# Kernel optimization log

Measured on AMD Instinct MI355X. Metric: run time of the kernel, lower is better.

Reference implementation:

```python
import jax, jax.numpy as jnp
import numpy as np

EPS = 1e-7
STRIDE = 1
PAD = 3


def _mantissa_map(v):
    # (|v|+eps) * 2^(-floor(log2(|v|+eps))) - 1  -> mantissa-1 in [0,1)
    a = jnp.abs(v) + EPS
    base = a * jnp.exp2(-jnp.floor(jnp.log2(a))) - 1.0
    # piecewise: >=0.5 -> (1+base)/2, else 1+base  (values in [0.75, 1.5))
    return jnp.where(base >= 0.5, (1.0 + base) * 0.5, 1.0 + base)


def _unfold(x, kH, kW, stride, pad, Ho, Wo):
    # im2col matching torch.nn.Unfold ordering (kernel position index = i*kW + j)
    xp = jnp.pad(x, ((0, 0), (0, 0), (pad, pad), (pad, pad)))
    cols = [xp[:, :, i:i + stride * Ho:stride, j:j + stride * Wo:stride]
            for i in range(kH) for j in range(kW)]
    return jnp.stack(cols, axis=-1)  # (B, C, Ho, Wo, kH*kW)


def setup_inputs() -> dict:
    key = jax.random.key(0)
    k1, k2 = jax.random.split(key)
    x = jax.random.normal(k1, (4, 192, 56, 56), dtype=jnp.float32)
    weight = jax.random.normal(k2, (192, 1, 7, 7), dtype=jnp.float32) * 0.1
    return {"x": x, "weight": weight}


def reference(x, weight):
    B, C, H, W = x.shape
    _, _, kH, kW = weight.shape
    Ho = (H + 2 * PAD - kH) // STRIDE + 1
    Wo = (W + 2 * PAD - kW) // STRIDE + 1
    KK = kH * kW

    # mantissa factors
    m2 = _mantissa_map(weight).reshape(C, KK)[None, :, None, None, :]  # (1,C,1,1,KK)
    m1 = _unfold(_mantissa_map(x), kH, kW, STRIDE, PAD, Ho, Wo)        # (B,C,Ho,Wo,KK)
    # zeros come only from unfold's zero padding; map them to 1 (then 0 after -1)
    m1 = jnp.where(m1 == 0.0, 1.0, m1) - 1.0
    m2 = m2 - 1.0

    factor = (m1 + m2 + 1.0) / ((m1 + 1.0) * (m2 + 1.0))
    factor = jnp.where(jnp.isfinite(factor), factor, 1.0)

    q_x = _unfold(x, kH, kW, STRIDE, PAD, Ho, Wo)          # (B,C,Ho,Wo,KK)
    w = weight.reshape(C, KK)[None, :, None, None, :]       # (1,C,1,1,KK)
    q_y = jnp.sum(factor * (q_x * w), axis=-1)              # (B,C,Ho,Wo)
    return q_y.astype(jnp.float32)
```

## Files before the change

kernel.cpp:

```cpp
#include <hip/hip_runtime.h>

typedef float v2f __attribute__((ext_vector_type(2)));

#define EPS 1e-7f
#define TILE_H 14
#define RY 7
#define LDS_ROWS 20
#define LDS_COLS 64

__device__ __forceinline__ float mant_map(float v) {
    float a = fabsf(v) + EPS;
    unsigned int bi = __float_as_uint(a);
    float m = __uint_as_float((bi & 0x007FFFFFu) | 0x3F800000u);
    return (m >= 1.5f) ? 0.5f * m : m;
}

__global__ __launch_bounds__(64) void wprep_kernel(const float* __restrict__ w,
                                                   v2f* __restrict__ wt) {
    int t = blockIdx.x * 64 + threadIdx.x;
    if (t < 192 * 49) {
        float wv = w[t];
        float M2 = mant_map(wv);
        float B = wv / M2;
        wt[t] = (v2f){B, B * (M2 - 1.0f)};
    }
}

__global__ __launch_bounds__(128) void wconv_kernel(const float* __restrict__ x,
                                                    const v2f* __restrict__ wtab,
                                                    float* __restrict__ out) {
    __shared__ v2f sp[LDS_ROWS][LDS_COLS];

    const int tx = threadIdx.x;
    const int ty = threadIdx.y;
    const int tid = ty * 64 + tx;
    const int tile = blockIdx.x;
    const int c = blockIdx.y;
    const int b = blockIdx.z;

    const int y0 = tile * TILE_H;
    const long plane = (long)(b * 192 + c) * (56 * 56);
    const float* xp = x + plane;
    const v2f* wt = wtab + c * 49;

    for (int idx = tid; idx < LDS_ROWS * LDS_COLS; idx += 128) {
        int r = idx >> 6, lc = idx & 63;
        int ir = y0 - 3 + r, ic = lc - 3;
        float u = 0.0f;
        if (ir >= 0 && ir < 56 && ic >= 0 && ic < 56)
            u = xp[ir * 56 + ic];
        float v = u * __builtin_amdgcn_rcpf(mant_map(u));
        sp[r][lc] = (v2f){u, v};
    }
    __syncthreads();

    if (tx < 56) {
        v2f acc[RY];
        #pragma unroll
        for (int r = 0; r < RY; ++r) acc[r] = (v2f){0.f, 0.f};
        const int rb = ty * RY;

        #pragma unroll
        for (int ir = 0; ir < RY + 6; ++ir) {
            v2f p[7];
            #pragma unroll
            for (int j = 0; j < 7; ++j) p[j] = sp[rb + ir][tx + j];
            #pragma unroll
            for (int ry = 0; ry < RY; ++ry) {
                if (ir - ry >= 0 && ir - ry <= 6) {
                    const v2f* wr = wt + (ir - ry) * 7;
                    #pragma unroll
                    for (int j = 0; j < 7; ++j)
                        acc[ry] += p[j] * wr[j];
                }
            }
        }

        #pragma unroll
        for (int ry = 0; ry < RY; ++ry)
            out[plane + (y0 + rb + ry) * 56 + tx] = acc[ry].x + acc[ry].y;
    }
}

extern "C" void kernel_launch(void* const* d_in, const int* in_sizes, int n_in,
                              void* d_out, int out_size, void* d_ws, size_t ws_size,
                              hipStream_t stream) {
    const float* x = (const float*)d_in[0];
    const float* w = (const float*)d_in[1];
    float* out = (float*)d_out;
    v2f* wt = (v2f*)d_ws;

    hipLaunchKernelGGL(wprep_kernel, dim3(147), dim3(64), 0, stream, w, wt);
    hipLaunchKernelGGL(wconv_kernel, dim3(4, 192, 4), dim3(64, 2), 0, stream, x, wt, out);
}
```

Baseline: 72.56 us.

## Process whole plane per block with two output columns per thread

Each block now loads the full padded 62x64 plane into LDS and handles all 56 rows with 8 row-groups, rather than splitting each plane into four 14-row tiles. Each thread computes two adjacent output columns, reading LDS with 16-byte vector loads and writing float2 results, so each weight load feeds two FMAs. This removes the halo reloads between row tiles and cuts LDS reads per output. In exchange the grid shrinks from 3072 to 768 blocks and each block uses about 31 KB of LDS, which can lower occupancy and leave 4 of every 32 lanes idle.

```diff
diff --git a/kernel.cpp b/kernel.cpp
--- a/kernel.cpp
+++ b/kernel.cpp
@@ -1,11 +1,10 @@
 #include <hip/hip_runtime.h>
 
 typedef float v2f __attribute__((ext_vector_type(2)));
+typedef float v4f __attribute__((ext_vector_type(4)));
 
 #define EPS 1e-7f
-#define TILE_H 14
-#define RY 7
-#define LDS_ROWS 20
+#define LDS_ROWS 62
 #define LDS_COLS 64
 
 __device__ __forceinline__ float mant_map(float v) {
@@ -26,26 +25,24 @@
     }
 }
 
-__global__ __launch_bounds__(128) void wconv_kernel(const float* __restrict__ x,
+__global__ __launch_bounds__(256) void wconv_kernel(const float* __restrict__ x,
                                                     const v2f* __restrict__ wtab,
                                                     float* __restrict__ out) {
     __shared__ v2f sp[LDS_ROWS][LDS_COLS];
 
-    const int tx = threadIdx.x;
+    const int lx = threadIdx.x;
     const int ty = threadIdx.y;
-    const int tid = ty * 64 + tx;
-    const int tile = blockIdx.x;
-    const int c = blockIdx.y;
-    const int b = blockIdx.z;
+    const int tid = ty * 32 + lx;
+    const int c = blockIdx.x;
+    const int b = blockIdx.y;
 
-    const int y0 = tile * TILE_H;
     const long plane = (long)(b * 192 + c) * (56 * 56);
     const float* xp = x + plane;
     const v2f* wt = wtab + c * 49;
 
-    for (int idx = tid; idx < LDS_ROWS * LDS_COLS; idx += 128) {
+    for (int idx = tid; idx < LDS_ROWS * LDS_COLS; idx += 256) {
         int r = idx >> 6, lc = idx & 63;
-        int ir = y0 - 3 + r, ic = lc - 3;
+        int ir = r - 3, ic = lc - 3;
         float u = 0.0f;
         if (ir >= 0 && ir < 56 && ic >= 0 && ic < 56)
             u = xp[ir * 56 + ic];
@@ -54,31 +51,41 @@
     }
     __syncthreads();
 
-    if (tx < 56) {
-        v2f acc[RY];
+    if (lx < 28) {
+        const int x0 = lx * 2;
+        const int rb = ty * 7;
+
+        v2f a0[7], a1[7];
         #pragma unroll
-        for (int r = 0; r < RY; ++r) acc[r] = (v2f){0.f, 0.f};
-        const int rb = ty * RY;
+        for (int r = 0; r < 7; ++r) { a0[r] = (v2f){0.f, 0.f}; a1[r] = (v2f){0.f, 0.f}; }
 
         #pragma unroll
-        for (int ir = 0; ir < RY + 6; ++ir) {
-            v2f p[7];
+        for (int ir2 = 0; ir2 < 13; ++ir2) {
+            const v4f* q = (const v4f*)&sp[rb + ir2][x0];
+            v4f q0 = q[0], q1 = q[1], q2 = q[2], q3 = q[3];
+            float t[16] = {q0.x, q0.y, q0.z, q0.w, q1.x, q1.y, q1.z, q1.w,
+                           q2.x, q2.y, q2.z, q2.w, q3.x, q3.y, q3.z, q3.w};
+
             #pragma unroll
-            for (int j = 0; j < 7; ++j) p[j] = sp[rb + ir][tx + j];
-            #pragma unroll
-            for (int ry = 0; ry < RY; ++ry) {
-                if (ir - ry >= 0 && ir - ry <= 6) {
-                    const v2f* wr = wt + (ir - ry) * 7;
+            for (int ry = 0; ry < 7; ++ry) {
+                const int i = ir2 - ry;
+                if (i >= 0 && i <= 6) {
+                    const v2f* wr = wt + i * 7;
                     #pragma unroll
-                    for (int j = 0; j < 7; ++j)
-                        acc[ry] += p[j] * wr[j];
+                    for (int j = 0; j < 7; ++j) {
+                        v2f wc = wr[j];
+                        a0[ry] += (v2f){t[2 * j],     t[2 * j + 1]} * wc;
+                        a1[ry] += (v2f){t[2 * j + 2], t[2 * j + 3]} * wc;
+                    }
                 }
             }
         }
 
         #pragma unroll
-        for (int ry = 0; ry < RY; ++ry)
-            out[plane + (y0 + rb + ry) * 56 + tx] = acc[ry].x + acc[ry].y;
+        for (int ry = 0; ry < 7; ++ry) {
+            float2 o = make_float2(a0[ry].x + a0[ry].y, a1[ry].x + a1[ry].y);
+            *(float2*)&out[plane + (rb + ry) * 56 + x0] = o;
+        }
     }
 }
 
@@ -91,5 +98,5 @@
     v2f* wt = (v2f*)d_ws;
 
     hipLaunchKernelGGL(wprep_kernel, dim3(147), dim3(64), 0, stream, w, wt);
-    hipLaunchKernelGGL(wconv_kernel, dim3(4, 192, 4), dim3(64, 2), 0, stream, x, wt, out);
+    hipLaunchKernelGGL(wconv_kernel, dim3(192, 4), dim3(32, 8), 0, stream, x, wt, out);
 }
```

Result: no change. 73.75 us (+1.6%).
